# Optimization experiments

Measured on AMD Instinct MI355X. Metric: run time of the kernel, lower is better.

The kernel has to match this reference:

```python
import jax, jax.numpy as jnp
import numpy as np

GROUPS = 32
EPS = 1e-5


def group_norm(x, w, b):
    B, C, H, W = x.shape
    xg = x.reshape(B, GROUPS, C // GROUPS, H, W)
    mu = xg.mean(axis=(2, 3, 4), keepdims=True)
    var = xg.var(axis=(2, 3, 4), keepdims=True)
    xn = ((xg - mu) / jnp.sqrt(var + EPS)).reshape(B, C, H, W)
    return xn * w[None, :, None, None] + b[None, :, None, None]


def setup_inputs() -> dict:
    key = jax.random.key(0)
    ks = jax.random.split(key, 4)
    B, C, H, W = 8, 512, 32, 32
    x = jax.random.normal(ks[0], (B, C, H, W), dtype=jnp.float32)
    gn_w = jnp.ones((C,), dtype=jnp.float32)
    gn_b = jnp.zeros((C,), dtype=jnp.float32)
    # 1x1 conv weights, scaled like typical init for numerical sanity
    qkv_w = jax.random.normal(ks[1], (3 * C, C), dtype=jnp.float32) * (1.0 / np.sqrt(C))
    proj_w = jax.random.normal(ks[2], (C, C), dtype=jnp.float32) * (1.0 / np.sqrt(C))
    proj_b = jnp.zeros((C,), dtype=jnp.float32)
    return {"x": x, "gn_w": gn_w, "gn_b": gn_b, "qkv_w": qkv_w,
            "proj_w": proj_w, "proj_b": proj_b, "num_heads": 8}


def reference(x, gn_w, gn_b, qkv_w, proj_w, proj_b, num_heads):
    B, C, H, W = x.shape
    N = H * W
    head_dim = C // num_heads
    xn = group_norm(x, gn_w, gn_b)
    # 1x1 conv == channel matmul: (B, 3C, N)
    qkv = jnp.einsum('oc,bcn->bon', qkv_w, xn.reshape(B, C, N))
    # faithful to torch: reshape to (B*nh, 3*hd, N) then chunk into thirds
    qkv = qkv.reshape(B * num_heads, 3 * head_dim, N)
    q, k, v = jnp.split(qkv, 3, axis=1)  # each (B*nh, hd, N)
    scale = 1.0 / np.sqrt(np.sqrt(head_dim))
    attn = jax.nn.softmax(jnp.einsum('bct,bcs->bts', q * scale, k * scale), axis=-1)
    h = jnp.einsum('bts,bcs->bct', attn, v)  # (B*nh, hd, N)
    h = h.reshape(B, C, N)
    out = jnp.einsum('oc,bcn->bon', proj_w, h) + proj_b[None, :, None]
    return out.reshape(B, C, H, W) + x
```

## Files before the change

### kernel.cpp

```cpp
#include <hip/hip_runtime.h>

#define B_ 8
#define C_ 512
#define N_ 1024
#define GROUPS_ 32
#define CPG_ 16
#define NH_ 8
#define HD_ 64

typedef _Float16 half8 __attribute__((ext_vector_type(8)));
typedef _Float16 half2v __attribute__((ext_vector_type(2)));
typedef float f32x4 __attribute__((ext_vector_type(4)));
typedef float f32x16 __attribute__((ext_vector_type(16)));

#define QSCALE 0.18033688011112042f
#define THR_LOG2 11.0f

__global__ __launch_bounds__(256) void pack_weights(
    const float* __restrict__ qkv_w, const float* __restrict__ proj_w,
    _Float16* __restrict__ qkw, _Float16* __restrict__ vw,
    _Float16* __restrict__ pw) {
  const int R = blockIdx.x * 4 + (threadIdx.x >> 6);
  const int k = (threadIdx.x & 63) * 8;
  const float* src;
  _Float16* dst;
  float sc = 1.f;
  if (R < 1024) {
    const int head = R >> 7, r = R & 127;
    src = qkv_w + (size_t)(head * 192 + r) * 512;
    if (r < 64) sc = QSCALE;
    dst = qkw + (size_t)R * 512;
  } else if (R < 1536) {
    const int vr = R - 1024;
    const int head = vr >> 6, c = vr & 63;
    src = qkv_w + (size_t)(head * 192 + 128 + c) * 512;
    dst = vw + (size_t)vr * 512;
  } else {
    src = proj_w + (size_t)(R - 1536) * 512;
    dst = pw + (size_t)(R - 1536) * 512;
  }
  const float4 v0 = *reinterpret_cast<const float4*>(src + k);
  const float4 v1 = *reinterpret_cast<const float4*>(src + k + 4);
  _Float16 h[8] = {(_Float16)(v0.x * sc), (_Float16)(v0.y * sc),
                   (_Float16)(v0.z * sc), (_Float16)(v0.w * sc),
                   (_Float16)(v1.x * sc), (_Float16)(v1.y * sc),
                   (_Float16)(v1.z * sc), (_Float16)(v1.w * sc)};
  *reinterpret_cast<float4*>(dst + k) = *reinterpret_cast<float4*>(h);
}

__global__ __launch_bounds__(256) void gn_stats(const float* __restrict__ x,
                                                float2* __restrict__ stats) {
  const int bg = blockIdx.x;
  const int b = bg / GROUPS_, g = bg % GROUPS_;
  const float* xp = x + ((size_t)b * C_ + (size_t)g * CPG_) * N_;
  const int tid = threadIdx.x;
  const int total = CPG_ * N_;

  float s = 0.f, ss = 0.f;
  for (int i = tid * 4; i < total; i += 1024) {
    const float4 v = *reinterpret_cast<const float4*>(xp + i);
    s += v.x + v.y + v.z + v.w;
    ss += v.x * v.x + v.y * v.y + v.z * v.z + v.w * v.w;
  }
#pragma unroll
  for (int off = 32; off > 0; off >>= 1) {
    s += __shfl_down(s, off);
    ss += __shfl_down(ss, off);
  }
  __shared__ float red[8];
  if ((tid & 63) == 0) { red[tid >> 6] = s; red[4 + (tid >> 6)] = ss; }
  __syncthreads();
  if (tid == 0) {
    s = red[0] + red[1] + red[2] + red[3];
    ss = red[4] + red[5] + red[6] + red[7];
    const float inv = 1.0f / (float)total;
    const float mu = s * inv;
    const float var = ss * inv - mu * mu;
    stats[bg] = make_float2(mu, rsqrtf(var + 1e-5f));
  }
}

__global__ __launch_bounds__(256) void gn_norm(const float* __restrict__ x,
                                               const float* __restrict__ gw,
                                               const float* __restrict__ gb,
                                               const float2* __restrict__ stats,
                                               _Float16* __restrict__ xnT) {
  const int n0 = blockIdx.x * 16;
  const int b = blockIdx.y;
  __shared__ _Float16 T[16][520];
  __shared__ float wsh[512], bsh[512];
  const int tid = threadIdx.x;
  for (int c = tid; c < 512; c += 256) {
    const float2 st = stats[b * 32 + (c >> 4)];
    const float wv = gw[c] * st.y;
    wsh[c] = wv;
    bsh[c] = gb[c] - st.x * wv;
  }
  __syncthreads();
  {
    const int n = tid & 15;
    const int cb = tid >> 4;
    const float* xb = x + (size_t)b * C_ * N_ + n0 + n;
#pragma unroll
    for (int i = 0; i < 32; ++i) {
      const int c = i * 16 + cb;
      T[n][c] = (_Float16)(xb[(size_t)c * N_] * wsh[c] + bsh[c]);
    }
  }
  __syncthreads();
  const int row = tid >> 4;
  const int seg = tid & 15;
  _Float16* dst = &xnT[((size_t)b * N_ + n0 + row) * C_ + seg * 32];
  const _Float16* srcp = &T[row][seg * 32];
  *reinterpret_cast<float4*>(dst) = *reinterpret_cast<const float4*>(srcp);
  *reinterpret_cast<float4*>(dst + 8) = *reinterpret_cast<const float4*>(srcp + 8);
  *reinterpret_cast<float4*>(dst + 16) = *reinterpret_cast<const float4*>(srcp + 16);
  *reinterpret_cast<float4*>(dst + 24) = *reinterpret_cast<const float4*>(srcp + 24);
}

template <bool OUT_HALF, bool EPI>
__global__ __launch_bounds__(256) void gemm_tn(
    const _Float16* __restrict__ A, long strideAb,
    const _Float16* __restrict__ Bm, long strideBb,
    void* __restrict__ D, long strideDb, int ldd, int K,
    const float* __restrict__ bias, const float* __restrict__ resid,
    long strideRb) {
  const int bc0 = blockIdx.x * 128;
  const int ar0 = blockIdx.y * 128;
  const int b = blockIdx.z;
  const _Float16* Ab = A + (size_t)b * strideAb;
  const _Float16* Bb = Bm + (size_t)b * strideBb;

  __shared__ _Float16 As[128][40];
  __shared__ _Float16 Bs[128][40];

  const int tid = threadIdx.x;
  const int lane = tid & 63;
  const int wid = tid >> 6;
  const int war = (wid >> 1) * 64;
  const int wbc = (wid & 1) * 64;
  const int lg = lane >> 4;
  const int lr = lane & 15;

  const int srow = tid >> 1;
  const int skoff = (tid & 1) * 16;

  f32x4 acc[4][4] = {};

  for (int k0 = 0; k0 < K; k0 += 32) {
    __syncthreads();
    const float4 av0 = *reinterpret_cast<const float4*>(
        &Ab[(size_t)(ar0 + srow) * K + k0 + skoff]);
    const float4 av1 = *reinterpret_cast<const float4*>(
        &Ab[(size_t)(ar0 + srow) * K + k0 + skoff + 8]);
    const float4 bv0 = *reinterpret_cast<const float4*>(
        &Bb[(size_t)(bc0 + srow) * K + k0 + skoff]);
    const float4 bv1 = *reinterpret_cast<const float4*>(
        &Bb[(size_t)(bc0 + srow) * K + k0 + skoff + 8]);
    *reinterpret_cast<float4*>(&As[srow][skoff]) = av0;
    *reinterpret_cast<float4*>(&As[srow][skoff + 8]) = av1;
    *reinterpret_cast<float4*>(&Bs[srow][skoff]) = bv0;
    *reinterpret_cast<float4*>(&Bs[srow][skoff + 8]) = bv1;
    __syncthreads();

    half8 af[4], bf[4];
#pragma unroll
    for (int i = 0; i < 4; ++i)
      af[i] = *reinterpret_cast<const half8*>(&As[war + i * 16 + lr][lg * 8]);
#pragma unroll
    for (int j = 0; j < 4; ++j)
      bf[j] = *reinterpret_cast<const half8*>(&Bs[wbc + j * 16 + lr][lg * 8]);
#pragma unroll
    for (int i = 0; i < 4; ++i)
#pragma unroll
      for (int j = 0; j < 4; ++j)
        acc[i][j] = __builtin_amdgcn_mfma_f32_16x16x32_f16(af[i], bf[j],
                                                           acc[i][j], 0, 0, 0);
  }

  if (OUT_HALF) {
    _Float16* Dp = (_Float16*)D + (size_t)b * strideDb;
#pragma unroll
    for (int i = 0; i < 4; ++i)
#pragma unroll
      for (int r = 0; r < 4; ++r) {
        const int row = ar0 + war + i * 16 + lg * 4 + r;
#pragma unroll
        for (int j = 0; j < 4; ++j) {
          const int col = bc0 + wbc + j * 16 + lr;
          Dp[(size_t)row * ldd + col] = (_Float16)acc[i][j][r];
        }
      }
  }
  if (EPI) {
    float* Dp = (float*)D + (size_t)b * strideDb;
    const float* Rp = resid + (size_t)b * strideRb;
#pragma unroll
    for (int i = 0; i < 4; ++i)
#pragma unroll
      for (int r = 0; r < 4; ++r) {
        const int row = ar0 + war + i * 16 + lg * 4 + r;
        const float bv = bias[row];
#pragma unroll
        for (int j = 0; j < 4; ++j) {
          const int col = bc0 + wbc + j * 16 + lr;
          const size_t off = (size_t)row * ldd + col;
          Dp[off] = acc[i][j][r] + bv + Rp[off];
        }
      }
  }
}

__global__ __launch_bounds__(256, 1) void attn_mfma(
    const _Float16* __restrict__ qkT, const _Float16* __restrict__ vT,
    _Float16* __restrict__ hT) {
  const int qb = blockIdx.x * 256;
  const int bh = blockIdx.y;
  const int b = bh >> 3, head = bh & 7;
  const int tid = threadIdx.x;
  const int lane = tid & 63;
  const int w = tid >> 6;
  const int l31 = lane & 31;
  const int lg2 = lane >> 5;

  __shared__ _Float16 Ks[64][72];
  __shared__ _Float16 Vs[64][72];

  const size_t qkbase = (size_t)b * N_ * 1024;

  half8 bfq[2][4];
#pragma unroll
  for (int jt = 0; jt < 2; ++jt)
#pragma unroll
    for (int kc = 0; kc < 4; ++kc)
      bfq[jt][kc] = *reinterpret_cast<const half8*>(
          &qkT[qkbase + (size_t)(qb + w * 64 + jt * 32 + l31) * 1024 +
               head * 128 + kc * 16 + lg2 * 8]);

  const int sr = tid >> 2;
  const int sc = (tid & 3) * 16;
  const _Float16* kp0 = qkT + qkbase + (size_t)sr * 1024 + head * 128 + 64 + sc;
  const _Float16* vp0 = vT + ((size_t)bh * 64 + sr) * 1024 + sc;

  float4 kreg0 = *reinterpret_cast<const float4*>(kp0);
  float4 kreg1 = *reinterpret_cast<const float4*>(kp0 + 8);
  float4 vreg0 = *reinterpret_cast<const float4*>(vp0);
  float4 vreg1 = *reinterpret_cast<const float4*>(vp0 + 8);

  f32x16 oacc[2][2];
#pragma unroll
  for (int jt = 0; jt < 2; ++jt)
#pragma unroll
    for (int ct = 0; ct < 2; ++ct)
#pragma unroll
      for (int r = 0; r < 16; ++r) oacc[jt][ct][r] = 0.f;
  float m_run[2] = {-1e30f, -1e30f};
  float l_run[2] = {0.f, 0.f};

  for (int t = 0; t < 16; ++t) {
    __syncthreads();
    *reinterpret_cast<float4*>(&Ks[sr][sc]) = kreg0;
    *reinterpret_cast<float4*>(&Ks[sr][sc + 8]) = kreg1;
    *reinterpret_cast<float4*>(&Vs[sr][sc]) = vreg0;
    *reinterpret_cast<float4*>(&Vs[sr][sc + 8]) = vreg1;
    __syncthreads();
    {
      const int sbn = (t < 15) ? (t + 1) * 64 : 960;
      kreg0 = *reinterpret_cast<const float4*>(kp0 + (size_t)sbn * 1024);
      kreg1 = *reinterpret_cast<const float4*>(kp0 + (size_t)sbn * 1024 + 8);
      vreg0 = *reinterpret_cast<const float4*>(vp0 + sbn);
      vreg1 = *reinterpret_cast<const float4*>(vp0 + sbn + 8);
    }

    f32x16 sacc[2][2];
#pragma unroll
    for (int jt = 0; jt < 2; ++jt)
#pragma unroll
      for (int st = 0; st < 2; ++st)
#pragma unroll
        for (int r = 0; r < 16; ++r) sacc[jt][st][r] = 0.f;
#pragma unroll
    for (int st = 0; st < 2; ++st)
#pragma unroll
      for (int kc = 0; kc < 4; ++kc) {
        const half8 af = *reinterpret_cast<const half8*>(
            &Ks[st * 32 + l31][kc * 16 + lg2 * 8]);
        sacc[0][st] = __builtin_amdgcn_mfma_f32_32x32x16_f16(
            af, bfq[0][kc], sacc[0][st], 0, 0, 0);
        sacc[1][st] = __builtin_amdgcn_mfma_f32_32x32x16_f16(
            af, bfq[1][kc], sacc[1][st], 0, 0, 0);
      }

    half8 pa[2][4];
#pragma unroll
    for (int jt = 0; jt < 2; ++jt) {
      float mt = -1e30f;
#pragma unroll
      for (int st = 0; st < 2; ++st)
#pragma unroll
        for (int r = 0; r < 16; ++r) mt = fmaxf(mt, sacc[jt][st][r]);
      mt = fmaxf(mt, __shfl_xor(mt, 32));
      if (!__all(mt <= m_run[jt] + THR_LOG2)) {
        const float mn = fmaxf(m_run[jt], mt);
        const float alpha = exp2f(m_run[jt] - mn);
        m_run[jt] = mn;
        l_run[jt] *= alpha;
#pragma unroll
        for (int r = 0; r < 16; ++r) {
          const int qrow = (r & 3) + 8 * (r >> 2) + 4 * lg2;
          const float ar = __shfl(alpha, qrow);
          oacc[jt][0][r] *= ar;
          oacc[jt][1][r] *= ar;
        }
      }
      const float mr = m_run[jt];
      float ps = 0.f;
#pragma unroll
      for (int st = 0; st < 2; ++st)
#pragma unroll
        for (int r = 0; r < 16; ++r) {
          const float p = exp2f(sacc[jt][st][r] - mr);
          sacc[jt][st][r] = p;
          ps += p;
        }
      ps += __shfl_xor(ps, 32);
      l_run[jt] += ps;

      unsigned int wo[2][8];
#pragma unroll
      for (int st = 0; st < 2; ++st)
#pragma unroll
        for (int m = 0; m < 8; ++m) {
          union { half2v h; unsigned int u; } cv;
          cv.h.x = (_Float16)sacc[jt][st][2 * m];
          cv.h.y = (_Float16)sacc[jt][st][2 * m + 1];
          wo[st][m] = cv.u;
        }
#pragma unroll
      for (int kc = 0; kc < 4; ++kc) {
        const int st = kc >> 1;
        const int base = 4 * (kc & 1);
        const unsigned int a0 = wo[st][base], a1 = wo[st][base + 1];
        const unsigned int a2 = wo[st][base + 2], a3 = wo[st][base + 3];
        const unsigned int x0 = __shfl_xor(a0, 32);
        const unsigned int x1 = __shfl_xor(a1, 32);
        const unsigned int x2 = __shfl_xor(a2, 32);
        const unsigned int x3 = __shfl_xor(a3, 32);
        union { unsigned int u[4]; half8 h; } fr;
        fr.u[0] = lg2 ? x2 : a0;
        fr.u[1] = lg2 ? x3 : a1;
        fr.u[2] = lg2 ? a2 : x0;
        fr.u[3] = lg2 ? a3 : x1;
        pa[jt][kc] = fr.h;
      }
    }

#pragma unroll
    for (int ct = 0; ct < 2; ++ct)
#pragma unroll
      for (int ks = 0; ks < 4; ++ks) {
        const half8 vf = *reinterpret_cast<const half8*>(
            &Vs[ct * 32 + l31][ks * 16 + lg2 * 8]);
        oacc[0][ct] = __builtin_amdgcn_mfma_f32_32x32x16_f16(
            pa[0][ks], vf, oacc[0][ct], 0, 0, 0);
        oacc[1][ct] = __builtin_amdgcn_mfma_f32_32x32x16_f16(
            pa[1][ks], vf, oacc[1][ct], 0, 0, 0);
      }
  }

  const size_t hbase = ((size_t)b * N_ + qb) * C_ + head * 64;
#pragma unroll
  for (int jt = 0; jt < 2; ++jt) {
    const float linv = 1.f / l_run[jt];
#pragma unroll
    for (int r = 0; r < 16; ++r) {
      const int qrow = (r & 3) + 8 * (r >> 2) + 4 * lg2;
      const float li = __shfl(linv, qrow);
      const size_t rowoff = hbase + (size_t)(w * 64 + jt * 32 + qrow) * C_;
#pragma unroll
      for (int ct = 0; ct < 2; ++ct)
        hT[rowoff + ct * 32 + l31] = (_Float16)(oacc[jt][ct][r] * li);
    }
  }
}

extern "C" void kernel_launch(void* const* d_in, const int* in_sizes, int n_in,
                              void* d_out, int out_size, void* d_ws,
                              size_t ws_size, hipStream_t stream) {
  const float* x = (const float*)d_in[0];
  const float* gn_w = (const float*)d_in[1];
  const float* gn_b = (const float*)d_in[2];
  const float* qkv_w = (const float*)d_in[3];
  const float* proj_w = (const float*)d_in[4];
  const float* proj_b = (const float*)d_in[5];
  float* out = (float*)d_out;

  char* ws = (char*)d_ws;
  const size_t MB = 1024 * 1024;
  _Float16* qkw = (_Float16*)(ws);
  _Float16* vw = (_Float16*)(ws + 1 * MB);
  _Float16* pw = (_Float16*)(ws + 3 * MB / 2);
  float2* stats = (float2*)(ws + 2 * MB);
  _Float16* xnT = (_Float16*)(ws + 3 * MB);
  _Float16* qkT = (_Float16*)(ws + 11 * MB);
  _Float16* vT = (_Float16*)(ws + 27 * MB);
  _Float16* hT = (_Float16*)(ws + 35 * MB);

  pack_weights<<<dim3(512), 256, 0, stream>>>(qkv_w, proj_w, qkw, vw, pw);
  gn_stats<<<dim3(B_ * GROUPS_), 256, 0, stream>>>(x, stats);
  gn_norm<<<dim3(64, B_), 256, 0, stream>>>(x, gn_w, gn_b, stats, xnT);
  gemm_tn<true, false><<<dim3(8, 8, B_), 256, 0, stream>>>(
      xnT, (long)N_ * C_, qkw, 0L, qkT, (long)N_ * 1024, 1024, C_,
      nullptr, nullptr, 0L);
  gemm_tn<true, false><<<dim3(8, 4, B_), 256, 0, stream>>>(
      vw, 0L, xnT, (long)N_ * C_, vT, (long)512 * 1024, 1024, C_,
      nullptr, nullptr, 0L);
  attn_mfma<<<dim3(N_ / 256, B_ * NH_), 256, 0, stream>>>(qkT, vT, hT);
  gemm_tn<false, true><<<dim3(8, 4, B_), 256, 0, stream>>>(
      pw, 0L, hT, (long)N_ * C_, out, (long)C_ * N_, N_, C_,
      proj_b, x, (long)C_ * N_);
}
```

Baseline: 193.3 us.

## Double-buffer GEMM with direct global-to-LDS loads, shrink attention tiles, fuse prep kernels

The GEMM now stages 64-wide K tiles into a double-buffered, XOR-swizzled LDS layout using global_load_lds, so the next tile's loads overlap the current MFMAs. Attention blocks now cover 128 queries instead of 256, which doubles the grid to raise occupancy, and MFMA sections get raised wave priority. The weight packing and group-norm stats kernels are merged into one launch. Each attention block still reloads the full K/V per head, so halving the query tile roughly doubles K/V traffic.

```diff
diff --git a/kernel.cpp b/kernel.cpp
--- a/kernel.cpp
+++ b/kernel.cpp
@@ -16,67 +16,72 @@
 #define QSCALE 0.18033688011112042f
 #define THR_LOG2 11.0f
 
-__global__ __launch_bounds__(256) void pack_weights(
+__device__ __forceinline__ void gload_lds16(const void* g, void* l) {
+  __builtin_amdgcn_global_load_lds(
+      (const __attribute__((address_space(1))) unsigned int*)g,
+      (__attribute__((address_space(3))) unsigned int*)l, 16, 0, 0);
+}
+
+__global__ __launch_bounds__(256) void prep(
     const float* __restrict__ qkv_w, const float* __restrict__ proj_w,
-    _Float16* __restrict__ qkw, _Float16* __restrict__ vw,
-    _Float16* __restrict__ pw) {
-  const int R = blockIdx.x * 4 + (threadIdx.x >> 6);
-  const int k = (threadIdx.x & 63) * 8;
-  const float* src;
-  _Float16* dst;
-  float sc = 1.f;
-  if (R < 1024) {
-    const int head = R >> 7, r = R & 127;
-    src = qkv_w + (size_t)(head * 192 + r) * 512;
-    if (r < 64) sc = QSCALE;
-    dst = qkw + (size_t)R * 512;
-  } else if (R < 1536) {
-    const int vr = R - 1024;
-    const int head = vr >> 6, c = vr & 63;
-    src = qkv_w + (size_t)(head * 192 + 128 + c) * 512;
-    dst = vw + (size_t)vr * 512;
+    const float* __restrict__ x, _Float16* __restrict__ qkw,
+    _Float16* __restrict__ vw, _Float16* __restrict__ pw,
+    float2* __restrict__ stats) {
+  const int tid = threadIdx.x;
+  if (blockIdx.x < 512) {
+    const int R = blockIdx.x * 4 + (tid >> 6);
+    const int k = (tid & 63) * 8;
+    const float* src;
+    _Float16* dst;
+    float sc = 1.f;
+    if (R < 1024) {
+      const int head = R >> 7, r = R & 127;
+      src = qkv_w + (size_t)(head * 192 + r) * 512;
+      if (r < 64) sc = QSCALE;
+      dst = qkw + (size_t)R * 512;
+    } else if (R < 1536) {
+      const int vr = R - 1024;
+      const int head = vr >> 6, c = vr & 63;
+      src = qkv_w + (size_t)(head * 192 + 128 + c) * 512;
+      dst = vw + (size_t)vr * 512;
+    } else {
+      src = proj_w + (size_t)(R - 1536) * 512;
+      dst = pw + (size_t)(R - 1536) * 512;
+    }
+    const float4 v0 = *reinterpret_cast<const float4*>(src + k);
+    const float4 v1 = *reinterpret_cast<const float4*>(src + k + 4);
+    _Float16 h[8] = {(_Float16)(v0.x * sc), (_Float16)(v0.y * sc),
+                     (_Float16)(v0.z * sc), (_Float16)(v0.w * sc),
+                     (_Float16)(v1.x * sc), (_Float16)(v1.y * sc),
+                     (_Float16)(v1.z * sc), (_Float16)(v1.w * sc)};
+    *reinterpret_cast<float4*>(dst + k) = *reinterpret_cast<float4*>(h);
   } else {
-    src = proj_w + (size_t)(R - 1536) * 512;
-    dst = pw + (size_t)(R - 1536) * 512;
-  }
-  const float4 v0 = *reinterpret_cast<const float4*>(src + k);
-  const float4 v1 = *reinterpret_cast<const float4*>(src + k + 4);
-  _Float16 h[8] = {(_Float16)(v0.x * sc), (_Float16)(v0.y * sc),
-                   (_Float16)(v0.z * sc), (_Float16)(v0.w * sc),
-                   (_Float16)(v1.x * sc), (_Float16)(v1.y * sc),
-                   (_Float16)(v1.z * sc), (_Float16)(v1.w * sc)};
-  *reinterpret_cast<float4*>(dst + k) = *reinterpret_cast<float4*>(h);
-}
-
-__global__ __launch_bounds__(256) void gn_stats(const float* __restrict__ x,
-                                                float2* __restrict__ stats) {
-  const int bg = blockIdx.x;
-  const int b = bg / GROUPS_, g = bg % GROUPS_;
-  const float* xp = x + ((size_t)b * C_ + (size_t)g * CPG_) * N_;
-  const int tid = threadIdx.x;
-  const int total = CPG_ * N_;
-
-  float s = 0.f, ss = 0.f;
-  for (int i = tid * 4; i < total; i += 1024) {
-    const float4 v = *reinterpret_cast<const float4*>(xp + i);
-    s += v.x + v.y + v.z + v.w;
-    ss += v.x * v.x + v.y * v.y + v.z * v.z + v.w * v.w;
-  }
-#pragma unroll
-  for (int off = 32; off > 0; off >>= 1) {
-    s += __shfl_down(s, off);
-    ss += __shfl_down(ss, off);
-  }
-  __shared__ float red[8];
-  if ((tid & 63) == 0) { red[tid >> 6] = s; red[4 + (tid >> 6)] = ss; }
-  __syncthreads();
-  if (tid == 0) {
-    s = red[0] + red[1] + red[2] + red[3];
-    ss = red[4] + red[5] + red[6] + red[7];
-    const float inv = 1.0f / (float)total;
-    const float mu = s * inv;
-    const float var = ss * inv - mu * mu;
-    stats[bg] = make_float2(mu, rsqrtf(var + 1e-5f));
+    const int bg = blockIdx.x - 512;
+    const int b = bg / GROUPS_, g = bg % GROUPS_;
+    const float* xp = x + ((size_t)b * C_ + (size_t)g * CPG_) * N_;
+    const int total = CPG_ * N_;
+    float s = 0.f, ss = 0.f;
+    for (int i = tid * 4; i < total; i += 1024) {
+      const float4 v = *reinterpret_cast<const float4*>(xp + i);
+      s += v.x + v.y + v.z + v.w;
+      ss += v.x * v.x + v.y * v.y + v.z * v.z + v.w * v.w;
+    }
+#pragma unroll
+    for (int off = 32; off > 0; off >>= 1) {
+      s += __shfl_down(s, off);
+      ss += __shfl_down(ss, off);
+    }
+    __shared__ float red[8];
+    if ((tid & 63) == 0) { red[tid >> 6] = s; red[4 + (tid >> 6)] = ss; }
+    __syncthreads();
+    if (tid == 0) {
+      s = red[0] + red[1] + red[2] + red[3];
+      ss = red[4] + red[5] + red[6] + red[7];
+      const float inv = 1.0f / (float)total;
+      const float mu = s * inv;
+      const float var = ss * inv - mu * mu;
+      stats[bg] = make_float2(mu, rsqrtf(var + 1e-5f));
+    }
   }
 }
 
@@ -119,7 +124,7 @@
 }
 
 template <bool OUT_HALF, bool EPI>
-__global__ __launch_bounds__(256) void gemm_tn(
+__global__ __launch_bounds__(256, 2) void gemm_tn(
     const _Float16* __restrict__ A, long strideAb,
     const _Float16* __restrict__ Bm, long strideBb,
     void* __restrict__ D, long strideDb, int ldd, int K,
@@ -131,8 +136,8 @@
   const _Float16* Ab = A + (size_t)b * strideAb;
   const _Float16* Bb = Bm + (size_t)b * strideBb;
 
-  __shared__ _Float16 As[128][40];
-  __shared__ _Float16 Bs[128][40];
+  __shared__ _Float16 As[2][128][64];
+  __shared__ _Float16 Bs[2][128][64];
 
   const int tid = threadIdx.x;
   const int lane = tid & 63;
@@ -142,41 +147,49 @@
   const int lg = lane >> 4;
   const int lr = lane & 15;
 
-  const int srow = tid >> 1;
-  const int skoff = (tid & 1) * 16;
+  const int srow = lane >> 3;
+  const int sgr = (lane & 7) ^ srow;
+
+#define STAGE(buf, koff)                                                     \
+  _Pragma("unroll") for (int i = 0; i < 4; ++i) {                            \
+    const int rb = (i * 4 + wid) * 8;                                        \
+    gload_lds16(&Ab[(size_t)(ar0 + rb + srow) * K + (koff) + sgr * 8],       \
+                &As[buf][rb][0]);                                            \
+    gload_lds16(&Bb[(size_t)(bc0 + rb + srow) * K + (koff) + sgr * 8],       \
+                &Bs[buf][rb][0]);                                            \
+  }
 
   f32x4 acc[4][4] = {};
 
-  for (int k0 = 0; k0 < K; k0 += 32) {
+  STAGE(0, 0)
+  __syncthreads();
+
+  const int nsteps = K >> 6;
+  int cur = 0;
+  for (int step = 0; step < nsteps; ++step) {
+    if (step + 1 < nsteps) { STAGE(cur ^ 1, (step + 1) << 6) }
+    const half8* Ah = reinterpret_cast<const half8*>(&As[cur][0][0]);
+    const half8* Bh = reinterpret_cast<const half8*>(&Bs[cur][0][0]);
+#pragma unroll
+    for (int kc = 0; kc < 2; ++kc) {
+      half8 af[4], bf[4];
+#pragma unroll
+      for (int i = 0; i < 4; ++i)
+        af[i] = Ah[(war + i * 16 + lr) * 8 + ((4 * kc + lg) ^ (lr & 7))];
+#pragma unroll
+      for (int j = 0; j < 4; ++j)
+        bf[j] = Bh[(wbc + j * 16 + lr) * 8 + ((4 * kc + lg) ^ (lr & 7))];
+#pragma unroll
+      for (int i = 0; i < 4; ++i)
+#pragma unroll
+        for (int j = 0; j < 4; ++j)
+          acc[i][j] = __builtin_amdgcn_mfma_f32_16x16x32_f16(af[i], bf[j],
+                                                             acc[i][j], 0, 0, 0);
+    }
     __syncthreads();
-    const float4 av0 = *reinterpret_cast<const float4*>(
-        &Ab[(size_t)(ar0 + srow) * K + k0 + skoff]);
-    const float4 av1 = *reinterpret_cast<const float4*>(
-        &Ab[(size_t)(ar0 + srow) * K + k0 + skoff + 8]);
-    const float4 bv0 = *reinterpret_cast<const float4*>(
-        &Bb[(size_t)(bc0 + srow) * K + k0 + skoff]);
-    const float4 bv1 = *reinterpret_cast<const float4*>(
-        &Bb[(size_t)(bc0 + srow) * K + k0 + skoff + 8]);
-    *reinterpret_cast<float4*>(&As[srow][skoff]) = av0;
-    *reinterpret_cast<float4*>(&As[srow][skoff + 8]) = av1;
-    *reinterpret_cast<float4*>(&Bs[srow][skoff]) = bv0;
-    *reinterpret_cast<float4*>(&Bs[srow][skoff + 8]) = bv1;
-    __syncthreads();
-
-    half8 af[4], bf[4];
-#pragma unroll
-    for (int i = 0; i < 4; ++i)
-      af[i] = *reinterpret_cast<const half8*>(&As[war + i * 16 + lr][lg * 8]);
-#pragma unroll
-    for (int j = 0; j < 4; ++j)
-      bf[j] = *reinterpret_cast<const half8*>(&Bs[wbc + j * 16 + lr][lg * 8]);
-#pragma unroll
-    for (int i = 0; i < 4; ++i)
-#pragma unroll
-      for (int j = 0; j < 4; ++j)
-        acc[i][j] = __builtin_amdgcn_mfma_f32_16x16x32_f16(af[i], bf[j],
-                                                           acc[i][j], 0, 0, 0);
-  }
+    cur ^= 1;
+  }
+#undef STAGE
 
   if (OUT_HALF) {
     _Float16* Dp = (_Float16*)D + (size_t)b * strideDb;
@@ -211,10 +224,10 @@
   }
 }
 
-__global__ __launch_bounds__(256, 1) void attn_mfma(
+__global__ __launch_bounds__(256, 2) void attn_mfma(
     const _Float16* __restrict__ qkT, const _Float16* __restrict__ vT,
     _Float16* __restrict__ hT) {
-  const int qb = blockIdx.x * 256;
+  const int qb = blockIdx.x * 128;
   const int bh = blockIdx.y;
   const int b = bh >> 3, head = bh & 7;
   const int tid = threadIdx.x;
@@ -228,14 +241,12 @@
 
   const size_t qkbase = (size_t)b * N_ * 1024;
 
-  half8 bfq[2][4];
-#pragma unroll
-  for (int jt = 0; jt < 2; ++jt)
-#pragma unroll
-    for (int kc = 0; kc < 4; ++kc)
-      bfq[jt][kc] = *reinterpret_cast<const half8*>(
-          &qkT[qkbase + (size_t)(qb + w * 64 + jt * 32 + l31) * 1024 +
-               head * 128 + kc * 16 + lg2 * 8]);
+  half8 bfq[4];
+#pragma unroll
+  for (int kc = 0; kc < 4; ++kc)
+    bfq[kc] = *reinterpret_cast<const half8*>(
+        &qkT[qkbase + (size_t)(qb + w * 32 + l31) * 1024 + head * 128 +
+             kc * 16 + lg2 * 8]);
 
   const int sr = tid >> 2;
   const int sc = (tid & 3) * 16;
@@ -247,15 +258,12 @@
   float4 vreg0 = *reinterpret_cast<const float4*>(vp0);
   float4 vreg1 = *reinterpret_cast<const float4*>(vp0 + 8);
 
-  f32x16 oacc[2][2];
-#pragma unroll
-  for (int jt = 0; jt < 2; ++jt)
-#pragma unroll
-    for (int ct = 0; ct < 2; ++ct)
-#pragma unroll
-      for (int r = 0; r < 16; ++r) oacc[jt][ct][r] = 0.f;
-  float m_run[2] = {-1e30f, -1e30f};
-  float l_run[2] = {0.f, 0.f};
+  f32x16 oacc[2];
+#pragma unroll
+  for (int ct = 0; ct < 2; ++ct)
+#pragma unroll
+    for (int r = 0; r < 16; ++r) oacc[ct][r] = 0.f;
+  float m_run = -1e30f, l_run = 0.f;
 
   for (int t = 0; t < 16; ++t) {
     __syncthreads();
@@ -272,68 +280,65 @@
       vreg1 = *reinterpret_cast<const float4*>(vp0 + sbn + 8);
     }
 
-    f32x16 sacc[2][2];
-#pragma unroll
-    for (int jt = 0; jt < 2; ++jt)
-#pragma unroll
-      for (int st = 0; st < 2; ++st)
-#pragma unroll
-        for (int r = 0; r < 16; ++r) sacc[jt][st][r] = 0.f;
+    f32x16 sacc[2];
+#pragma unroll
+    for (int st = 0; st < 2; ++st)
+#pragma unroll
+      for (int r = 0; r < 16; ++r) sacc[st][r] = 0.f;
+    __builtin_amdgcn_s_setprio(1);
 #pragma unroll
     for (int st = 0; st < 2; ++st)
 #pragma unroll
       for (int kc = 0; kc < 4; ++kc) {
         const half8 af = *reinterpret_cast<const half8*>(
             &Ks[st * 32 + l31][kc * 16 + lg2 * 8]);
-        sacc[0][st] = __builtin_amdgcn_mfma_f32_32x32x16_f16(
-            af, bfq[0][kc], sacc[0][st], 0, 0, 0);
-        sacc[1][st] = __builtin_amdgcn_mfma_f32_32x32x16_f16(
-            af, bfq[1][kc], sacc[1][st], 0, 0, 0);
-      }
-
-    half8 pa[2][4];
-#pragma unroll
-    for (int jt = 0; jt < 2; ++jt) {
-      float mt = -1e30f;
-#pragma unroll
-      for (int st = 0; st < 2; ++st)
-#pragma unroll
-        for (int r = 0; r < 16; ++r) mt = fmaxf(mt, sacc[jt][st][r]);
-      mt = fmaxf(mt, __shfl_xor(mt, 32));
-      if (!__all(mt <= m_run[jt] + THR_LOG2)) {
-        const float mn = fmaxf(m_run[jt], mt);
-        const float alpha = exp2f(m_run[jt] - mn);
-        m_run[jt] = mn;
-        l_run[jt] *= alpha;
-#pragma unroll
-        for (int r = 0; r < 16; ++r) {
-          const int qrow = (r & 3) + 8 * (r >> 2) + 4 * lg2;
-          const float ar = __shfl(alpha, qrow);
-          oacc[jt][0][r] *= ar;
-          oacc[jt][1][r] *= ar;
-        }
-      }
-      const float mr = m_run[jt];
-      float ps = 0.f;
-#pragma unroll
-      for (int st = 0; st < 2; ++st)
-#pragma unroll
-        for (int r = 0; r < 16; ++r) {
-          const float p = exp2f(sacc[jt][st][r] - mr);
-          sacc[jt][st][r] = p;
-          ps += p;
-        }
-      ps += __shfl_xor(ps, 32);
-      l_run[jt] += ps;
-
+        sacc[st] = __builtin_amdgcn_mfma_f32_32x32x16_f16(af, bfq[kc],
+                                                          sacc[st], 0, 0, 0);
+      }
+    __builtin_amdgcn_s_setprio(0);
+
+    float mt = -1e30f;
+#pragma unroll
+    for (int st = 0; st < 2; ++st)
+#pragma unroll
+      for (int r = 0; r < 16; ++r) mt = fmaxf(mt, sacc[st][r]);
+    mt = fmaxf(mt, __shfl_xor(mt, 32));
+    if (!__all(mt <= m_run + THR_LOG2)) {
+      const float mn = fmaxf(m_run, mt);
+      const float alpha = exp2f(m_run - mn);
+      m_run = mn;
+      l_run *= alpha;
+#pragma unroll
+      for (int r = 0; r < 16; ++r) {
+        const int qrow = (r & 3) + 8 * (r >> 2) + 4 * lg2;
+        const float ar = __shfl(alpha, qrow);
+        oacc[0][r] *= ar;
+        oacc[1][r] *= ar;
+      }
+    }
+    const float mr = m_run;
+    float ps = 0.f;
+#pragma unroll
+    for (int st = 0; st < 2; ++st)
+#pragma unroll
+      for (int r = 0; r < 16; ++r) {
+        const float p = exp2f(sacc[st][r] - mr);
+        sacc[st][r] = p;
+        ps += p;
+      }
+    ps += __shfl_xor(ps, 32);
+    l_run += ps;
+
+    half8 pa[4];
+    {
       unsigned int wo[2][8];
 #pragma unroll
       for (int st = 0; st < 2; ++st)
 #pragma unroll
         for (int m = 0; m < 8; ++m) {
           union { half2v h; unsigned int u; } cv;
-          cv.h.x = (_Float16)sacc[jt][st][2 * m];
-          cv.h.y = (_Float16)sacc[jt][st][2 * m + 1];
+          cv.h.x = (_Float16)sacc[st][2 * m];
+          cv.h.y = (_Float16)sacc[st][2 * m + 1];
           wo[st][m] = cv.u;
         }
 #pragma unroll
@@ -351,36 +356,33 @@
         fr.u[1] = lg2 ? x3 : a1;
         fr.u[2] = lg2 ? a2 : x0;
         fr.u[3] = lg2 ? a3 : x1;
-        pa[jt][kc] = fr.h;
-      }
-    }
-
+        pa[kc] = fr.h;
+      }
+    }
+
+    __builtin_amdgcn_s_setprio(1);
 #pragma unroll
     for (int ct = 0; ct < 2; ++ct)
 #pragma unroll
       for (int ks = 0; ks < 4; ++ks) {
         const half8 vf = *reinterpret_cast<const half8*>(
             &Vs[ct * 32 + l31][ks * 16 + lg2 * 8]);
-        oacc[0][ct] = __builtin_amdgcn_mfma_f32_32x32x16_f16(
-            pa[0][ks], vf, oacc[0][ct], 0, 0, 0);
-        oacc[1][ct] = __builtin_amdgcn_mfma_f32_32x32x16_f16(
-            pa[1][ks], vf, oacc[1][ct], 0, 0, 0);
-      }
+        oacc[ct] = __builtin_amdgcn_mfma_f32_32x32x16_f16(pa[ks], vf,
+                                                          oacc[ct], 0, 0, 0);
+      }
+    __builtin_amdgcn_s_setprio(0);
   }
 
   const size_t hbase = ((size_t)b * N_ + qb) * C_ + head * 64;
-#pragma unroll
-  for (int jt = 0; jt < 2; ++jt) {
-    const float linv = 1.f / l_run[jt];
-#pragma unroll
-    for (int r = 0; r < 16; ++r) {
-      const int qrow = (r & 3) + 8 * (r >> 2) + 4 * lg2;
-      const float li = __shfl(linv, qrow);
-      const size_t rowoff = hbase + (size_t)(w * 64 + jt * 32 + qrow) * C_;
-#pragma unroll
-      for (int ct = 0; ct < 2; ++ct)
-        hT[rowoff + ct * 32 + l31] = (_Float16)(oacc[jt][ct][r] * li);
-    }
+  const float linv = 1.f / l_run;
+#pragma unroll
+  for (int r = 0; r < 16; ++r) {
+    const int qrow = (r & 3) + 8 * (r >> 2) + 4 * lg2;
+    const float li = __shfl(linv, qrow);
+    const size_t rowoff = hbase + (size_t)(w * 32 + qrow) * C_;
+#pragma unroll
+    for (int ct = 0; ct < 2; ++ct)
+      hT[rowoff + ct * 32 + l31] = (_Float16)(oacc[ct][r] * li);
   }
 }
 
@@ -406,8 +408,7 @@
   _Float16* vT = (_Float16*)(ws + 27 * MB);
   _Float16* hT = (_Float16*)(ws + 35 * MB);
 
-  pack_weights<<<dim3(512), 256, 0, stream>>>(qkv_w, proj_w, qkw, vw, pw);
-  gn_stats<<<dim3(B_ * GROUPS_), 256, 0, stream>>>(x, stats);
+  prep<<<dim3(768), 256, 0, stream>>>(qkv_w, proj_w, x, qkw, vw, pw, stats);
   gn_norm<<<dim3(64, B_), 256, 0, stream>>>(x, gn_w, gn_b, stats, xnT);
   gemm_tn<true, false><<<dim3(8, 8, B_), 256, 0, stream>>>(
       xnT, (long)N_ * C_, qkw, 0L, qkT, (long)N_ * 1024, 1024, C_,
@@ -415,7 +416,7 @@
   gemm_tn<true, false><<<dim3(8, 4, B_), 256, 0, stream>>>(
       vw, 0L, xnT, (long)N_ * C_, vT, (long)512 * 1024, 1024, C_,
       nullptr, nullptr, 0L);
-  attn_mfma<<<dim3(N_ / 256, B_ * NH_), 256, 0, stream>>>(qkT, vT, hT);
+  attn_mfma<<<dim3(N_ / 128, B_ * NH_), 256, 0, stream>>>(qkT, vT, hT);
   gemm_tn<false, true><<<dim3(8, 4, B_), 256, 0, stream>>>(
       pw, 0L, hT, (long)N_ * C_, out, (long)C_ * N_, N_, C_,
       proj_b, x, (long)C_ * N_);
```

Result: faster. 171.1 us (-11.5%).
